# Performance work log

Measured on AMD Instinct MI355X. Metric: run time of the kernel, lower is better.

The kernel has to match this reference:

```python
import jax, jax.numpy as jnp
import numpy as np

B_, H_, N_, L_ = 4, 512, 64, 2048  # batch, d_model, d_state/2 (conj pairs), seq len


def setup_inputs() -> dict:
    key = jax.random.key(0)
    ks = jax.random.split(key, 8)
    x = jax.random.normal(ks[0], (B_, H_, L_), jnp.float32)
    ln_w = jnp.ones((H_,), jnp.float32)
    ln_b = jnp.zeros((H_,), jnp.float32)
    # S4D-style init: dt log-uniform in [1e-3, 1e-1], A = -1/2 + i*pi*n (S4D-Lin)
    log_dt = jax.random.uniform(ks[1], (H_,), jnp.float32) * (np.log(0.1) - np.log(0.001)) + np.log(0.001)
    log_A_real = jnp.broadcast_to(jnp.log(jnp.float32(0.5)), (H_, N_))
    A_imag = jnp.broadcast_to(np.pi * jnp.arange(N_, dtype=np.float32), (H_, N_))
    B_re = jnp.ones((H_, N_), jnp.float32)
    B_im = jnp.zeros((H_, N_), jnp.float32)
    # 2 kernel channels for bidirectional
    C_re = jax.random.normal(ks[2], (2, H_, N_), jnp.float32) * (0.5 ** 0.5)
    C_im = jax.random.normal(ks[3], (2, H_, N_), jnp.float32) * (0.5 ** 0.5)
    D = jax.random.normal(ks[4], (H_,), jnp.float32)
    W_out = jax.random.normal(ks[5], (H_, H_), jnp.float32) / np.sqrt(H_)
    b_out = jnp.zeros((H_,), jnp.float32)
    return dict(x=x, ln_w=ln_w, ln_b=ln_b, log_dt=log_dt, log_A_real=log_A_real,
                A_imag=A_imag, B_re=B_re, B_im=B_im, C_re=C_re, C_im=C_im,
                D=D, W_out=W_out, b_out=b_out)


def _s4_layer(x, ln_w, ln_b, log_dt, log_A_real, A_imag, B_re, B_im, C_re, C_im, D, W_out, b_out):
    Bb, H, L = x.shape
    # ---- pre-norm LayerNorm over channel dim (module transposes to (B,L,H)) ----
    zt = x.transpose(0, 2, 1)                          # (B, L, H)
    mu = zt.mean(-1, keepdims=True)
    var = jnp.mean((zt - mu) ** 2, -1, keepdims=True)
    zt = (zt - mu) * jax.lax.rsqrt(var + 1e-5) * ln_w + ln_b
    z = zt.transpose(0, 2, 1)                          # (B, H, L)
    # ---- S4 diagonal SSM kernel, ZOH discretization, 2 channels (bidirectional) ----
    dt = jnp.exp(log_dt)[:, None]                      # (H, 1)
    A = -jnp.exp(log_A_real) + 1j * A_imag             # (H, N)
    dtA = A * dt                                       # (H, N)
    dB = (B_re + 1j * B_im) * (jnp.exp(dtA) - 1.0) / A # (H, N) discretized B
    CB = (C_re + 1j * C_im) * dB                       # (2, H, N)
    V = jnp.exp(dtA[:, :, None] * jnp.arange(L))       # (H, N, L) Vandermonde exp(l*dt*A)
    k = 2.0 * jnp.real(jnp.einsum('chn,hnl->chl', CB, V))  # (2, H, L)
    # ---- bidirectional: causal + flipped anticausal kernel, length 2L ----
    zpad = jnp.zeros_like(k[0])
    kb = jnp.concatenate([k[0], zpad], -1) + jnp.concatenate([zpad, k[1][:, ::-1]], -1)  # (H, 2L)
    # ---- FFT convolution ----
    k_f = jnp.fft.rfft(kb, n=2 * L)                    # (H, L+1)
    u_f = jnp.fft.rfft(z, n=2 * L)                     # (B, H, L+1)
    y = jnp.fft.irfft(u_f * k_f, n=2 * L)[..., :L]     # (B, H, L)
    y = y + z * D[:, None]                             # skip connection D*u
    y = jax.nn.gelu(y)                                 # default S4 activation
    y = jnp.einsum('oh,bhl->bol', W_out, y) + b_out[:, None]  # output linear (Conv1d k=1)
    return y + x                                       # residual of S4Layer


def reference(x, ln_w, ln_b, log_dt, log_A_real, A_imag, B_re, B_im, C_re, C_im, D, W_out, b_out):
    return _s4_layer(x, ln_w, ln_b, log_dt, log_A_real, A_imag, B_re, B_im, C_re, C_im, D, W_out, b_out)
```

## Files before the change

kernel.cpp:

```cpp
#include <hip/hip_runtime.h>
#include <math.h>

#define Bq 4
#define Hq 512
#define Nq 64
#define Lq 2048
#define PARAM (Hq*Nq)

__global__ void prep_kernel(const float* __restrict__ log_dt,
                            const float* __restrict__ log_A_real,
                            const float* __restrict__ A_imag,
                            const float* __restrict__ B_re, const float* __restrict__ B_im,
                            const float* __restrict__ C_re, const float* __restrict__ C_im,
                            float* __restrict__ wr_, float* __restrict__ wi_,
                            float* __restrict__ a0, float* __restrict__ b0,
                            float* __restrict__ a1, float* __restrict__ b1) {
    int idx = blockIdx.x * blockDim.x + threadIdx.x;
    if (idx >= PARAM) return;
    int h = idx >> 6;
    float dt = expf(log_dt[h]);
    float Ar = -expf(log_A_real[idx]);
    float Ai = A_imag[idx];
    float er = expf(Ar * dt);
    float wr = er * cosf(Ai * dt);
    float wi = er * sinf(Ai * dt);
    wr_[idx] = wr; wi_[idx] = wi;
    float mr = wr - 1.0f, mi = wi;
    float den = Ar * Ar + Ai * Ai;
    float qr = (mr * Ar + mi * Ai) / den;
    float qi = (mi * Ar - mr * Ai) / den;
    float Br = B_re[idx], Bi = B_im[idx];
    float dBr = Br * qr - Bi * qi;
    float dBi = Br * qi + Bi * qr;
    float cr = C_re[idx], ci = C_im[idx];
    a0[idx] =  2.0f * (cr * dBr - ci * dBi);
    b0[idx] = -2.0f * (cr * dBi + ci * dBr);
    cr = C_re[PARAM + idx]; ci = C_im[PARAM + idx];
    a1[idx] =  2.0f * (cr * dBr - ci * dBi);
    b1[idx] = -2.0f * (cr * dBi + ci * dBr);
}

__global__ __launch_bounds__(256)
void ln_kernel(const float* __restrict__ x, const float* __restrict__ lnw,
               const float* __restrict__ lnb, float* __restrict__ z) {
    int blk = blockIdx.x;
    int b  = blk / (Lq / 16);
    int l0 = (blk % (Lq / 16)) * 16;
    int tx = threadIdx.x & 15;
    int ty = threadIdx.x >> 4;
    const float* xb = x + (size_t)b * Hq * Lq;
    float s = 0.f, s2 = 0.f;
    for (int h = ty; h < Hq; h += 16) {
        float v = xb[h * Lq + l0 + tx];
        s += v; s2 += v * v;
    }
    __shared__ float rs_[16][17], r2_[16][17], mu_s[16], sg_s[16];
    rs_[ty][tx] = s; r2_[ty][tx] = s2;
    __syncthreads();
    if (ty == 0) {
        float a = 0.f, c = 0.f;
        #pragma unroll
        for (int i = 0; i < 16; ++i) { a += rs_[i][tx]; c += r2_[i][tx]; }
        float mu = a * (1.0f / Hq);
        float var = c * (1.0f / Hq) - mu * mu;
        mu_s[tx] = mu;
        sg_s[tx] = rsqrtf(var + 1e-5f);
    }
    __syncthreads();
    float mu = mu_s[tx], rs = sg_s[tx];
    float* zb = z + (size_t)b * Hq * Lq;
    for (int h = ty; h < Hq; h += 16) {
        float v = xb[h * Lq + l0 + tx];
        zb[h * Lq + l0 + tx] = (v - mu) * rs * lnw[h] + lnb[h];
    }
}

template <int DIR>
__device__ __forceinline__ void scan_body(const float* __restrict__ zz,
                                          float* __restrict__ yout,
                                          float wr, float wi, float a, float b,
                                          float (*tile)[33], float* zbuf, int n) {
    float sr = 0.f, si = 0.f;
    for (int q0 = 0; q0 < Lq; q0 += 32) {
        if (n < 32) zbuf[n] = zz[DIR ? (Lq - 1 - q0 - n) : (q0 + n)];
        __syncthreads();
        float p[32];
        #pragma unroll
        for (int k = 0; k < 32; ++k) {
            float zt = zbuf[k];
            if (DIR == 0) {
                float t1 = fmaf(wi, si, -zt);
                float t2 = wi * sr;
                sr = fmaf(wr, sr, -t1);
                si = fmaf(wr, si, t2);
                p[k] = fmaf(a, sr, b * si);
            } else {
                p[k] = fmaf(a, sr, b * si);
                float t1 = fmaf(wi, si, -zt);
                float t2 = wi * sr;
                sr = fmaf(wr, sr, -t1);
                si = fmaf(wr, si, t2);
            }
        }
        #pragma unroll
        for (int k = 0; k < 32; ++k) tile[n][k] = p[k];
        __syncthreads();
        int tloc = n & 31, ih = n >> 5;
        float acc = 0.f;
        #pragma unroll
        for (int j = 0; j < 32; ++j) acc += tile[ih * 32 + j][tloc];
        acc += __shfl_xor(acc, 32, 64);
        if (n < 32) yout[DIR ? (Lq - 1 - q0 - n) : (q0 + n)] = acc;
    }
}

__global__ __launch_bounds__(64)
void scan_kernel(const float* __restrict__ z,
                 const float* __restrict__ wr_, const float* __restrict__ wi_,
                 const float* __restrict__ a0, const float* __restrict__ b0,
                 const float* __restrict__ a1, const float* __restrict__ b1,
                 float* __restrict__ y0, float* __restrict__ y1) {
    int bh  = blockIdx.x;
    int dir = blockIdx.y;
    int h = bh & (Hq - 1);
    int n = threadIdx.x;
    int pidx = h * Nq + n;
    float wr = wr_[pidx], wi = wi_[pidx];
    __shared__ float tile[64][33];
    __shared__ float zbuf[32];
    const float* zz = z + (size_t)bh * Lq;
    if (dir == 0) {
        scan_body<0>(zz, y0 + (size_t)bh * Lq, wr, wi, a0[pidx], b0[pidx], tile, zbuf, n);
    } else {
        scan_body<1>(zz, y1 + (size_t)bh * Lq, wr, wi, a1[pidx], b1[pidx], tile, zbuf, n);
    }
}

__global__ __launch_bounds__(256)
void act_kernel(float4* __restrict__ y0, const float4* __restrict__ y1,
                const float4* __restrict__ z, const float* __restrict__ D) {
    int i4 = blockIdx.x * 256 + threadIdx.x;
    int h = (i4 >> 9) & (Hq - 1);
    float d = D[h];
    float4 v0 = y0[i4], v1 = y1[i4], vz = z[i4];
    float vv[4] = { v0.x + v1.x + d * vz.x, v0.y + v1.y + d * vz.y,
                    v0.z + v1.z + d * vz.z, v0.w + v1.w + d * vz.w };
    #pragma unroll
    for (int i = 0; i < 4; ++i) {
        float v = vv[i];
        float t = tanhf(0.7978845608028654f * (v + 0.044715f * v * v * v));
        vv[i] = 0.5f * v * (1.0f + t);
    }
    float4 r; r.x = vv[0]; r.y = vv[1]; r.z = vv[2]; r.w = vv[3];
    y0[i4] = r;
}

__global__ __launch_bounds__(256)
void gemm_kernel(const float* __restrict__ u, const float* __restrict__ W,
                 const float* __restrict__ bias, const float* __restrict__ x,
                 float* __restrict__ out) {
    int l0 = blockIdx.x * 64;
    int o0 = blockIdx.y * 128;
    int b  = blockIdx.z;
    int tid = threadIdx.x;
    __shared__ float Ws[16][129];
    __shared__ float Us[16][65];
    const float* ub = u + (size_t)b * Hq * Lq;
    float acc[8][4] = {};
    int wo = tid >> 4, wl = tid & 15;
    for (int k0 = 0; k0 < Hq; k0 += 16) {
        {
            int j  = tid & 15;
            int ib = tid >> 4;
            #pragma unroll
            for (int r = 0; r < 8; ++r) {
                int i = ib + 16 * r;
                Ws[j][i] = W[(size_t)(o0 + i) * Hq + k0 + j];
            }
            int li = tid & 63;
            int jb = tid >> 6;
            #pragma unroll
            for (int r = 0; r < 4; ++r) {
                int j2 = jb + 4 * r;
                Us[j2][li] = ub[(size_t)(k0 + j2) * Lq + l0 + li];
            }
        }
        __syncthreads();
        #pragma unroll
        for (int j = 0; j < 16; ++j) {
            float av[8], bv[4];
            #pragma unroll
            for (int i = 0; i < 8; ++i) av[i] = Ws[j][8 * wo + i];
            #pragma unroll
            for (int i = 0; i < 4; ++i) bv[i] = Us[j][4 * wl + i];
            #pragma unroll
            for (int io = 0; io < 8; ++io)
                #pragma unroll
                for (int il = 0; il < 4; ++il)
                    acc[io][il] = fmaf(av[io], bv[il], acc[io][il]);
        }
        __syncthreads();
    }
    #pragma unroll
    for (int io = 0; io < 8; ++io) {
        int o = o0 + 8 * wo + io;
        float bo = bias[o];
        size_t base = ((size_t)b * Hq + o) * Lq + l0 + 4 * wl;
        const float4 xr = *(const float4*)(x + base);
        float4 r;
        r.x = acc[io][0] + bo + xr.x;
        r.y = acc[io][1] + bo + xr.y;
        r.z = acc[io][2] + bo + xr.z;
        r.w = acc[io][3] + bo + xr.w;
        *(float4*)(out + base) = r;
    }
}

extern "C" void kernel_launch(void* const* d_in, const int* in_sizes, int n_in,
                              void* d_out, int out_size, void* d_ws, size_t ws_size,
                              hipStream_t stream) {
    (void)in_sizes; (void)n_in; (void)out_size; (void)ws_size;
    const float* x          = (const float*)d_in[0];
    const float* ln_w       = (const float*)d_in[1];
    const float* ln_b       = (const float*)d_in[2];
    const float* log_dt     = (const float*)d_in[3];
    const float* log_A_real = (const float*)d_in[4];
    const float* A_imag     = (const float*)d_in[5];
    const float* B_re       = (const float*)d_in[6];
    const float* B_im       = (const float*)d_in[7];
    const float* C_re       = (const float*)d_in[8];
    const float* C_im       = (const float*)d_in[9];
    const float* Dv         = (const float*)d_in[10];
    const float* W          = (const float*)d_in[11];
    const float* b_out      = (const float*)d_in[12];
    float* out = (float*)d_out;
    float* ws  = (float*)d_ws;

    float* wr = ws;
    float* wi = ws + PARAM;
    float* a0 = ws + 2 * PARAM;
    float* b0 = ws + 3 * PARAM;
    float* a1 = ws + 4 * PARAM;
    float* b1 = ws + 5 * PARAM;
    float* z  = ws + 6 * PARAM;
    float* y0 = z  + (size_t)Bq * Hq * Lq;
    float* y1 = y0 + (size_t)Bq * Hq * Lq;

    prep_kernel<<<PARAM / 256, 256, 0, stream>>>(log_dt, log_A_real, A_imag,
                                                 B_re, B_im, C_re, C_im,
                                                 wr, wi, a0, b0, a1, b1);
    ln_kernel<<<Bq * (Lq / 16), 256, 0, stream>>>(x, ln_w, ln_b, z);
    scan_kernel<<<dim3(Bq * Hq, 2), 64, 0, stream>>>(z, wr, wi, a0, b0, a1, b1, y0, y1);
    act_kernel<<<(Bq * Hq * Lq / 4) / 256, 256, 0, stream>>>((float4*)y0, (const float4*)y1,
                                                             (const float4*)z, Dv);
    gemm_kernel<<<dim3(Lq / 64, Hq / 128, Bq), 256, 0, stream>>>(y0, W, b_out, x, out);
}
```

Before: 325.9 us.

## Chunk the SSM recurrence across sequence with a two-pass carry-combine scan

Splits each sequence into four chunks. A new local kernel computes the end state of each of the first three chunks, and the scan kernel combines those chunk states into carry-in states using precomputed powers w^512, w^1024 and w^1536, which are computed in double precision in the prep kernel. Each chunk's scan then runs in its own wavefront of a 256-thread block, which shortens the serial dependency chain by a factor of four and raises parallelism. The per-step reduction now uses wave-local LDS tiles with wave barriers instead of block syncs, and z is read directly with float4 loads. The cost is an extra kernel and a redundant pass over z, plus some precision risk when the chunk carries are combined.

After: 373.6 us. 1.15x slower.

```diff
diff --git a/kernel.cpp b/kernel.cpp
--- a/kernel.cpp
+++ b/kernel.cpp
@@ -6,6 +6,10 @@
 #define Nq 64
 #define Lq 2048
 #define PARAM (Hq*Nq)
+#define BH   (Bq*Hq)
+#define CCH  4
+#define LC   (Lq/CCH)
+static_assert(Lq == CCH*LC, "chunking");
 
 __global__ void prep_kernel(const float* __restrict__ log_dt,
                             const float* __restrict__ log_A_real,
@@ -14,7 +18,8 @@
                             const float* __restrict__ C_re, const float* __restrict__ C_im,
                             float* __restrict__ wr_, float* __restrict__ wi_,
                             float* __restrict__ a0, float* __restrict__ b0,
-                            float* __restrict__ a1, float* __restrict__ b1) {
+                            float* __restrict__ a1, float* __restrict__ b1,
+                            float* __restrict__ wpr, float* __restrict__ wpi) {
     int idx = blockIdx.x * blockDim.x + threadIdx.x;
     if (idx >= PARAM) return;
     int h = idx >> 6;
@@ -38,6 +43,18 @@
     cr = C_re[PARAM + idx]; ci = C_im[PARAM + idx];
     a1[idx] =  2.0f * (cr * dBr - ci * dBi);
     b1[idx] = -2.0f * (cr * dBi + ci * dBr);
+    double pr = (double)wr, pq = (double)wi;
+    #pragma unroll
+    for (int s = 0; s < 9; ++s) {
+        double nr = pr*pr - pq*pq;
+        double ni = 2.0*pr*pq;
+        pr = nr; pq = ni;
+    }
+    wpr[idx] = (float)pr;  wpi[idx] = (float)pq;
+    double p2r = pr*pr - pq*pq, p2i = 2.0*pr*pq;
+    wpr[PARAM + idx] = (float)p2r; wpi[PARAM + idx] = (float)p2i;
+    double p3r = p2r*pr - p2i*pq, p3i = p2r*pq + p2i*pr;
+    wpr[2*PARAM + idx] = (float)p3r; wpi[2*PARAM + idx] = (float)p3i;
 }
 
 __global__ __launch_bounds__(256)
@@ -75,65 +92,132 @@
     }
 }
 
+__device__ __forceinline__ void sstep(float& sr, float& si, float wr, float wi, float zt) {
+    float t1 = fmaf(wi, si, -zt);
+    float t2 = wi * sr;
+    sr = fmaf(wr, sr, -t1);
+    si = fmaf(wr, si, t2);
+}
+
+#define SSTEP4(qq)  do { sstep(sr,si,wr,wi,(qq).x); sstep(sr,si,wr,wi,(qq).y); \
+                         sstep(sr,si,wr,wi,(qq).z); sstep(sr,si,wr,wi,(qq).w); } while(0)
+#define SSTEP4R(qq) do { sstep(sr,si,wr,wi,(qq).w); sstep(sr,si,wr,wi,(qq).z); \
+                         sstep(sr,si,wr,wi,(qq).y); sstep(sr,si,wr,wi,(qq).x); } while(0)
+
+__global__ __launch_bounds__(256, 8)
+void local_kernel(const float* __restrict__ z,
+                  const float* __restrict__ wr_, const float* __restrict__ wi_,
+                  float* __restrict__ slocal) {
+    int wv = threadIdx.x >> 6;
+    int n  = threadIdx.x & 63;
+    int bh = blockIdx.x * 4 + wv;
+    int dir = blockIdx.y;
+    int c  = blockIdx.z;
+    int h  = bh & (Hq - 1);
+    int pidx = h * Nq + n;
+    float wr = wr_[pidx], wi = wi_[pidx];
+    const float* zz = z + (size_t)bh * Lq;
+    float sr = 0.f, si = 0.f;
+    int tau0 = c * LC;
+    if (dir == 0) {
+        const float4* zp = (const float4*)(zz + tau0);
+        for (int jj = 0; jj < LC; jj += 16) {
+            float4 q0 = zp[0], q1 = zp[1], q2 = zp[2], q3 = zp[3];
+            zp += 4;
+            SSTEP4(q0); SSTEP4(q1); SSTEP4(q2); SSTEP4(q3);
+        }
+    } else {
+        for (int jj = 0; jj < LC; jj += 16) {
+            const float4* zp = (const float4*)(zz + Lq - tau0 - jj - 16);
+            float4 q0 = zp[0], q1 = zp[1], q2 = zp[2], q3 = zp[3];
+            SSTEP4R(q3); SSTEP4R(q2); SSTEP4R(q1); SSTEP4R(q0);
+        }
+    }
+    float* out = slocal + ((size_t)(bh * 2 + dir) * (CCH - 1) + c) * 128;
+    out[n] = sr; out[64 + n] = si;
+}
+
 template <int DIR>
-__device__ __forceinline__ void scan_body(const float* __restrict__ zz,
-                                          float* __restrict__ yout,
-                                          float wr, float wi, float a, float b,
-                                          float (*tile)[33], float* zbuf, int n) {
-    float sr = 0.f, si = 0.f;
-    for (int q0 = 0; q0 < Lq; q0 += 32) {
-        if (n < 32) zbuf[n] = zz[DIR ? (Lq - 1 - q0 - n) : (q0 + n)];
-        __syncthreads();
-        float p[32];
+__device__ __forceinline__ void scan3_body(const float* __restrict__ zz,
+                                           float* __restrict__ yout,
+                                           float wr, float wi, float a, float b,
+                                           float sr, float si, int tau0, int n,
+                                           float (*tile)[17]) {
+    int g = n >> 4, tc = n & 15;
+    for (int q0 = 0; q0 < LC; q0 += 16) {
+        float4 q[4];
+        if (DIR == 0) {
+            const float4* zp = (const float4*)(zz + tau0 + q0);
+            q[0] = zp[0]; q[1] = zp[1]; q[2] = zp[2]; q[3] = zp[3];
+        } else {
+            const float4* zp = (const float4*)(zz + Lq - tau0 - q0 - 16);
+            q[0] = zp[0]; q[1] = zp[1]; q[2] = zp[2]; q[3] = zp[3];
+        }
         #pragma unroll
-        for (int k = 0; k < 32; ++k) {
-            float zt = zbuf[k];
+        for (int j = 0; j < 16; ++j) {
+            float zt;
             if (DIR == 0) {
-                float t1 = fmaf(wi, si, -zt);
-                float t2 = wi * sr;
-                sr = fmaf(wr, sr, -t1);
-                si = fmaf(wr, si, t2);
-                p[k] = fmaf(a, sr, b * si);
+                float4 qq = q[j >> 2];
+                zt = (j&3)==0 ? qq.x : (j&3)==1 ? qq.y : (j&3)==2 ? qq.z : qq.w;
             } else {
-                p[k] = fmaf(a, sr, b * si);
-                float t1 = fmaf(wi, si, -zt);
-                float t2 = wi * sr;
-                sr = fmaf(wr, sr, -t1);
-                si = fmaf(wr, si, t2);
+                float4 qq = q[3 - (j >> 2)];
+                zt = (j&3)==0 ? qq.w : (j&3)==1 ? qq.z : (j&3)==2 ? qq.y : qq.x;
             }
-        }
-        #pragma unroll
-        for (int k = 0; k < 32; ++k) tile[n][k] = p[k];
-        __syncthreads();
-        int tloc = n & 31, ih = n >> 5;
+            float p;
+            if (DIR == 0) { sstep(sr, si, wr, wi, zt); p = fmaf(a, sr, b * si); }
+            else          { p = fmaf(a, sr, b * si); sstep(sr, si, wr, wi, zt); }
+            tile[n][j] = p;
+        }
+        __builtin_amdgcn_wave_barrier();
         float acc = 0.f;
         #pragma unroll
-        for (int j = 0; j < 32; ++j) acc += tile[ih * 32 + j][tloc];
+        for (int r = 0; r < 16; ++r) acc += tile[g * 16 + r][tc];
+        acc += __shfl_xor(acc, 16, 64);
         acc += __shfl_xor(acc, 32, 64);
-        if (n < 32) yout[DIR ? (Lq - 1 - q0 - n) : (q0 + n)] = acc;
-    }
-}
-
-__global__ __launch_bounds__(64)
+        if (n < 16) {
+            int t = tau0 + q0 + n;
+            yout[DIR ? (Lq - 1 - t) : t] = acc;
+        }
+        __builtin_amdgcn_wave_barrier();
+    }
+}
+
+__global__ __launch_bounds__(256, 8)
 void scan_kernel(const float* __restrict__ z,
                  const float* __restrict__ wr_, const float* __restrict__ wi_,
                  const float* __restrict__ a0, const float* __restrict__ b0,
                  const float* __restrict__ a1, const float* __restrict__ b1,
+                 const float* __restrict__ wpr, const float* __restrict__ wpi,
+                 const float* __restrict__ slocal,
                  float* __restrict__ y0, float* __restrict__ y1) {
-    int bh  = blockIdx.x;
-    int dir = blockIdx.y;
+    __shared__ float tile[4][64][17];
+    int c = threadIdx.x >> 6;
+    int n = threadIdx.x & 63;
+    int bh = blockIdx.x, dir = blockIdx.y;
     int h = bh & (Hq - 1);
-    int n = threadIdx.x;
     int pidx = h * Nq + n;
     float wr = wr_[pidx], wi = wi_[pidx];
-    __shared__ float tile[64][33];
-    __shared__ float zbuf[32];
+    float sr = 0.f, si = 0.f;
+    const float* sl = slocal + (size_t)(bh * 2 + dir) * (CCH - 1) * 128;
+    for (int cp = 0; cp < c; ++cp) {
+        float lr = sl[cp * 128 + n], li = sl[cp * 128 + 64 + n];
+        int j = c - 1 - cp;
+        if (j == 0) { sr += lr; si += li; }
+        else {
+            float pr = wpr[(j - 1) * PARAM + pidx];
+            float pi = wpi[(j - 1) * PARAM + pidx];
+            sr += pr * lr - pi * li;
+            si += pr * li + pi * lr;
+        }
+    }
+    int tau0 = c * LC;
     const float* zz = z + (size_t)bh * Lq;
-    if (dir == 0) {
-        scan_body<0>(zz, y0 + (size_t)bh * Lq, wr, wi, a0[pidx], b0[pidx], tile, zbuf, n);
-    } else {
-        scan_body<1>(zz, y1 + (size_t)bh * Lq, wr, wi, a1[pidx], b1[pidx], tile, zbuf, n);
-    }
+    if (dir == 0)
+        scan3_body<0>(zz, y0 + (size_t)bh * Lq, wr, wi, a0[pidx], b0[pidx],
+                      sr, si, tau0, n, tile[c]);
+    else
+        scan3_body<1>(zz, y1 + (size_t)bh * Lq, wr, wi, a1[pidx], b1[pidx],
+                      sr, si, tau0, n, tile[c]);
 }
 
 __global__ __launch_bounds__(256)
@@ -236,21 +320,27 @@
     float* out = (float*)d_out;
     float* ws  = (float*)d_ws;
 
-    float* wr = ws;
-    float* wi = ws + PARAM;
-    float* a0 = ws + 2 * PARAM;
-    float* b0 = ws + 3 * PARAM;
-    float* a1 = ws + 4 * PARAM;
-    float* b1 = ws + 5 * PARAM;
-    float* z  = ws + 6 * PARAM;
-    float* y0 = z  + (size_t)Bq * Hq * Lq;
-    float* y1 = y0 + (size_t)Bq * Hq * Lq;
+    const size_t BHL = (size_t)Bq * Hq * Lq;
+    float* wr  = ws;
+    float* wi  = ws + PARAM;
+    float* a0  = ws + 2 * (size_t)PARAM;
+    float* b0  = ws + 3 * (size_t)PARAM;
+    float* a1  = ws + 4 * (size_t)PARAM;
+    float* b1  = ws + 5 * (size_t)PARAM;
+    float* wpr = ws + 6 * (size_t)PARAM;
+    float* wpi = ws + 9 * (size_t)PARAM;
+    float* z   = ws + 12 * (size_t)PARAM;
+    float* y0  = z  + BHL;
+    float* y1  = y0 + BHL;
+    float* slc = y1 + BHL;
 
     prep_kernel<<<PARAM / 256, 256, 0, stream>>>(log_dt, log_A_real, A_imag,
                                                  B_re, B_im, C_re, C_im,
-                                                 wr, wi, a0, b0, a1, b1);
+                                                 wr, wi, a0, b0, a1, b1, wpr, wpi);
     ln_kernel<<<Bq * (Lq / 16), 256, 0, stream>>>(x, ln_w, ln_b, z);
-    scan_kernel<<<dim3(Bq * Hq, 2), 64, 0, stream>>>(z, wr, wi, a0, b0, a1, b1, y0, y1);
+    local_kernel<<<dim3(BH / 4, 2, CCH - 1), 256, 0, stream>>>(z, wr, wi, slc);
+    scan_kernel<<<dim3(BH, 2), 256, 0, stream>>>(z, wr, wi, a0, b0, a1, b1,
+                                                 wpr, wpi, slc, y0, y1);
     act_kernel<<<(Bq * Hq * Lq / 4) / 256, 256, 0, stream>>>((float4*)y0, (const float4*)y1,
                                                              (const float4*)z, Dv);
     gemm_kernel<<<dim3(Lq / 64, Hq / 128, Bq), 256, 0, stream>>>(y0, W, b_out, x, out);
```

## Replace sequential SSM scan with chunked matmul-based scan

Applied to the files above, without the earlier changes.

Replaces the per-step recurrent scan over the full sequence with a chunked formulation. A delta kernel computes each chunk's state contribution as a matrix product with powers of the diagonal eigenvalues. A short inter-chunk scan then carries states across 32 chunks, and a y kernel combines the intra-chunk Toeplitz convolution with the carried-state contribution as a small GEMM. This removes the long serial dependency chain and exposes parallelism, at the cost of three kernel launches, an extra workspace buffer, and the numerical risk of power recurrences in float.

Measured after the change: 324.3 us. No clear change (-0.5%).

```diff
diff --git a/kernel.cpp b/kernel.cpp
--- a/kernel.cpp
+++ b/kernel.cpp
@@ -6,6 +6,9 @@
 #define Nq 64
 #define Lq 2048
 #define PARAM (Hq*Nq)
+#define T 64
+#define NC (Lq/T)
+#define NCOL 256
 
 __global__ void prep_kernel(const float* __restrict__ log_dt,
                             const float* __restrict__ log_A_real,
@@ -75,64 +78,238 @@
     }
 }
 
-template <int DIR>
-__device__ __forceinline__ void scan_body(const float* __restrict__ zz,
-                                          float* __restrict__ yout,
-                                          float wr, float wi, float a, float b,
-                                          float (*tile)[33], float* zbuf, int n) {
+
+__global__ __launch_bounds__(256)
+void delta_kernel(const float* __restrict__ z,
+                  const float* __restrict__ wr_, const float* __restrict__ wi_,
+                  float* __restrict__ buf) {
+    __shared__ float powc[64][64], pows[64][64];
+    __shared__ float Bs[64][68];
+    int h = blockIdx.x, ct = blockIdx.y;
+    int t = threadIdx.x;
+    if (t < 64) {
+        float wr = wr_[h*64+t], wi = wi_[h*64+t];
+        float c = 1.f, s = 0.f;
+        for (int d = 0; d < 64; ++d) {
+            powc[d][t] = c; pows[d][t] = s;
+            float nc = c*wr - s*wi, ns = c*wi + s*wr;
+            c = nc; s = ns;
+        }
+    }
+    {
+        int dir = ct >> 1;
+        int r = t >> 7, tt = t & 127;
+        int b = (ct & 1)*2 + r;
+        int l = tt * 16;
+        int c0 = l >> 6, j0 = l & 63;
+        const float* zb = z + ((size_t)b*Hq + h)*Lq;
+        int cc = r*32 + c0;
+        if (dir == 0) {
+            #pragma unroll
+            for (int q = 0; q < 4; ++q)
+                *(float4*)&Bs[cc][j0+4*q] = *(const float4*)(zb + c0*64 + j0 + 4*q);
+        } else {
+            #pragma unroll
+            for (int q = 0; q < 4; ++q) {
+                float4 v = *(const float4*)(zb + 2044 - c0*64 - (j0+4*q));
+                float4 w; w.x = v.w; w.y = v.z; w.z = v.y; w.w = v.x;
+                *(float4*)&Bs[cc][j0+4*q] = w;
+            }
+        }
+    }
+    __syncthreads();
+    int cg = t & 15, rg = t >> 4;
+    int n0 = 4*rg;
+    float aR[4][4] = {}, aI[4][4] = {};
+    #pragma unroll 4
+    for (int j = 0; j < 64; ++j) {
+        int d = 63 - j;
+        float4 pc = *(const float4*)&powc[d][n0];
+        float4 ps = *(const float4*)&pows[d][n0];
+        float bz[4];
+        #pragma unroll
+        for (int q = 0; q < 4; ++q) bz[q] = Bs[cg + 16*q][j];
+        #pragma unroll
+        for (int nn = 0; nn < 4; ++nn) {
+            float pcv = (&pc.x)[nn], psv = (&ps.x)[nn];
+            #pragma unroll
+            for (int q = 0; q < 4; ++q) {
+                aR[nn][q] = fmaf(pcv, bz[q], aR[nn][q]);
+                aI[nn][q] = fmaf(psv, bz[q], aI[nn][q]);
+            }
+        }
+    }
+    #pragma unroll
+    for (int q = 0; q < 4; ++q) {
+        int col = ct*64 + cg + 16*q;
+        float* dst = buf + ((size_t)h*NCOL + col)*128 + 2*n0;
+        float4 v1, v2;
+        v1.x = aR[0][q]; v1.y = aI[0][q]; v1.z = aR[1][q]; v1.w = aI[1][q];
+        v2.x = aR[2][q]; v2.y = aI[2][q]; v2.z = aR[3][q]; v2.w = aI[3][q];
+        *(float4*)dst = v1; *(float4*)(dst+4) = v2;
+    }
+}
+
+__global__ __launch_bounds__(256)
+void cscan_kernel(const float* __restrict__ wr_, const float* __restrict__ wi_,
+                  float* __restrict__ buf) {
+    int e = blockIdx.x*4 + (threadIdx.x >> 6);
+    int n = threadIdx.x & 63;
+    int h = e >> 3, dir = (e >> 2) & 1, b = e & 3;
+    float wr = wr_[h*64+n], wi = wi_[h*64+n];
+    double cr = wr, ci = wi;
+    #pragma unroll
+    for (int q = 0; q < 6; ++q) {
+        double nr = cr*cr - ci*ci, ni = 2.0*cr*ci;
+        cr = nr; ci = ni;
+    }
+    float tc = (float)cr, ts = (float)ci;
     float sr = 0.f, si = 0.f;
-    for (int q0 = 0; q0 < Lq; q0 += 32) {
-        if (n < 32) zbuf[n] = zz[DIR ? (Lq - 1 - q0 - n) : (q0 + n)];
+    float2* p = (float2*)(buf + ((size_t)h*NCOL + dir*128 + b*32)*128) + n;
+    float2 d = p[0];
+    for (int c = 0; c < NC; ++c) {
+        float2 dn;
+        if (c + 1 < NC) dn = p[(c+1)*64];
+        float2 s; s.x = sr; s.y = si;
+        p[c*64] = s;
+        float nr = fmaf(tc, sr, fmaf(-ts, si, d.x));
+        float ni = fmaf(ts, sr, fmaf(tc, si, d.y));
+        sr = nr; si = ni; d = dn;
+    }
+}
+
+__global__ __launch_bounds__(256)
+void y_kernel(const float* __restrict__ z,
+              const float* __restrict__ wr_, const float* __restrict__ wi_,
+              const float* __restrict__ a0, const float* __restrict__ b0,
+              const float* __restrict__ a1, const float* __restrict__ b1,
+              const float* __restrict__ buf,
+              float* __restrict__ y0, float* __restrict__ y1) {
+    __shared__ float powc[64][64], pows[64][64];
+    __shared__ float As[32][64];
+    __shared__ float Bs[64][36];
+    __shared__ float ks[64], as_[64], bs_[64];
+    int h = blockIdx.x, dir = blockIdx.y, ct = blockIdx.z;
+    int t = threadIdx.x;
+    const float* aa = dir ? a1 : a0;
+    const float* bb = dir ? b1 : b0;
+    if (t < 64) {
+        float wr = wr_[h*64+t], wi = wi_[h*64+t];
+        as_[t] = aa[h*64+t]; bs_[t] = bb[h*64+t];
+        float c, s;
+        if (dir == 0) { c = wr; s = wi; } else { c = 1.f; s = 0.f; }
+        for (int d = 0; d < 64; ++d) {
+            powc[d][t] = c; pows[d][t] = s;
+            float nc = c*wr - s*wi, ns = c*wi + s*wr;
+            c = nc; s = ns;
+        }
+    }
+    __syncthreads();
+    if (t < 64) {
+        int d = t;
+        float acc = 0.f;
+        if (dir == 0 && d == 0) {
+            for (int st = 0; st < 64; ++st) acc += as_[(st + d) & 63];
+        } else {
+            int row = (dir == 0) ? d - 1 : d;
+            for (int st = 0; st < 64; ++st) {
+                int n = (st + d) & 63;
+                acc = fmaf(as_[n], powc[row][n], acc);
+                acc = fmaf(bs_[n], pows[row][n], acc);
+            }
+        }
+        ks[d] = acc;
+    }
+    __syncthreads();
+    int tx = t & 15, ty = t >> 4;
+    float acc[4][4] = {};
+    for (int p = 0; p < 6; ++p) {
+        {
+            int kk = t & 31, ig = t >> 5;
+            if (p < 2) {
+                int j = 32*p + kk;
+                int off = (dir == 0) ? 0 : 1;
+                #pragma unroll
+                for (int ii = 0; ii < 8; ++ii) {
+                    int i = ig*8 + ii;
+                    int idx = i - j - off;
+                    As[kk][i] = (idx >= 0) ? ks[idx] : 0.f;
+                }
+            } else {
+                int m = 32*(p-2) + kk;
+                int n = m >> 1;
+                float av = as_[n], bv = bs_[n];
+                if ((m & 1) == 0) {
+                    #pragma unroll
+                    for (int ii = 0; ii < 8; ++ii) {
+                        int i = ig*8 + ii;
+                        As[kk][i] = fmaf(av, powc[i][n], bv*pows[i][n]);
+                    }
+                } else {
+                    #pragma unroll
+                    for (int ii = 0; ii < 8; ++ii) {
+                        int i = ig*8 + ii;
+                        As[kk][i] = fmaf(bv, powc[i][n], -av*pows[i][n]);
+                    }
+                }
+            }
+        }
+        {
+            int cc = t >> 2, q = t & 3;
+            int colg = ct*64 + cc;
+            int b = colg >> 5, c = colg & 31;
+            int kk0 = q*8;
+            if (p < 2) {
+                const float* zb = z + ((size_t)b*Hq + h)*Lq;
+                int j0 = 32*p + kk0;
+                if (dir == 0) {
+                    *(float4*)&Bs[cc][kk0]   = *(const float4*)(zb + c*64 + j0);
+                    *(float4*)&Bs[cc][kk0+4] = *(const float4*)(zb + c*64 + j0 + 4);
+                } else {
+                    float4 v = *(const float4*)(zb + 2044 - c*64 - j0);
+                    float4 w; w.x=v.w; w.y=v.z; w.z=v.y; w.w=v.x;
+                    *(float4*)&Bs[cc][kk0] = w;
+                    v = *(const float4*)(zb + 2044 - c*64 - (j0+4));
+                    w.x=v.w; w.y=v.z; w.z=v.y; w.w=v.x;
+                    *(float4*)&Bs[cc][kk0+4] = w;
+                }
+            } else {
+                int m0 = 32*(p-2) + kk0;
+                int col = dir*128 + colg;
+                const float* src = buf + ((size_t)h*NCOL + col)*128 + m0;
+                *(float4*)&Bs[cc][kk0]   = *(const float4*)src;
+                *(float4*)&Bs[cc][kk0+4] = *(const float4*)(src+4);
+            }
+        }
         __syncthreads();
-        float p[32];
-        #pragma unroll
-        for (int k = 0; k < 32; ++k) {
-            float zt = zbuf[k];
-            if (DIR == 0) {
-                float t1 = fmaf(wi, si, -zt);
-                float t2 = wi * sr;
-                sr = fmaf(wr, sr, -t1);
-                si = fmaf(wr, si, t2);
-                p[k] = fmaf(a, sr, b * si);
-            } else {
-                p[k] = fmaf(a, sr, b * si);
-                float t1 = fmaf(wi, si, -zt);
-                float t2 = wi * sr;
-                sr = fmaf(wr, sr, -t1);
-                si = fmaf(wr, si, t2);
-            }
-        }
-        #pragma unroll
-        for (int k = 0; k < 32; ++k) tile[n][k] = p[k];
+        #pragma unroll 8
+        for (int kk = 0; kk < 32; ++kk) {
+            float4 av = *(const float4*)&As[kk][4*tx];
+            float bv0 = Bs[4*ty+0][kk], bv1 = Bs[4*ty+1][kk];
+            float bv2 = Bs[4*ty+2][kk], bv3 = Bs[4*ty+3][kk];
+            #pragma unroll
+            for (int ii = 0; ii < 4; ++ii) {
+                float a = (&av.x)[ii];
+                acc[ii][0] = fmaf(a, bv0, acc[ii][0]);
+                acc[ii][1] = fmaf(a, bv1, acc[ii][1]);
+                acc[ii][2] = fmaf(a, bv2, acc[ii][2]);
+                acc[ii][3] = fmaf(a, bv3, acc[ii][3]);
+            }
+        }
         __syncthreads();
-        int tloc = n & 31, ih = n >> 5;
-        float acc = 0.f;
-        #pragma unroll
-        for (int j = 0; j < 32; ++j) acc += tile[ih * 32 + j][tloc];
-        acc += __shfl_xor(acc, 32, 64);
-        if (n < 32) yout[DIR ? (Lq - 1 - q0 - n) : (q0 + n)] = acc;
-    }
-}
-
-__global__ __launch_bounds__(64)
-void scan_kernel(const float* __restrict__ z,
-                 const float* __restrict__ wr_, const float* __restrict__ wi_,
-                 const float* __restrict__ a0, const float* __restrict__ b0,
-                 const float* __restrict__ a1, const float* __restrict__ b1,
-                 float* __restrict__ y0, float* __restrict__ y1) {
-    int bh  = blockIdx.x;
-    int dir = blockIdx.y;
-    int h = bh & (Hq - 1);
-    int n = threadIdx.x;
-    int pidx = h * Nq + n;
-    float wr = wr_[pidx], wi = wi_[pidx];
-    __shared__ float tile[64][33];
-    __shared__ float zbuf[32];
-    const float* zz = z + (size_t)bh * Lq;
-    if (dir == 0) {
-        scan_body<0>(zz, y0 + (size_t)bh * Lq, wr, wi, a0[pidx], b0[pidx], tile, zbuf, n);
-    } else {
-        scan_body<1>(zz, y1 + (size_t)bh * Lq, wr, wi, a1[pidx], b1[pidx], tile, zbuf, n);
+    }
+    #pragma unroll
+    for (int q = 0; q < 4; ++q) {
+        int colg = ct*64 + 4*ty + q;
+        int b = colg >> 5, c = colg & 31;
+        float4 v;
+        if (dir == 0) {
+            v.x = acc[0][q]; v.y = acc[1][q]; v.z = acc[2][q]; v.w = acc[3][q];
+            *(float4*)(y0 + ((size_t)b*Hq + h)*Lq + c*64 + 4*tx) = v;
+        } else {
+            v.x = acc[3][q]; v.y = acc[2][q]; v.z = acc[1][q]; v.w = acc[0][q];
+            *(float4*)(y1 + ((size_t)b*Hq + h)*Lq + 2044 - c*64 - 4*tx) = v;
+        }
     }
 }
 
@@ -148,8 +325,8 @@
     #pragma unroll
     for (int i = 0; i < 4; ++i) {
         float v = vv[i];
-        float t = tanhf(0.7978845608028654f * (v + 0.044715f * v * v * v));
-        vv[i] = 0.5f * v * (1.0f + t);
+        float tt = tanhf(0.7978845608028654f * (v + 0.044715f * v * v * v));
+        vv[i] = 0.5f * v * (1.0f + tt);
     }
     float4 r; r.x = vv[0]; r.y = vv[1]; r.z = vv[2]; r.w = vv[3];
     y0[i4] = r;
@@ -236,21 +413,26 @@
     float* out = (float*)d_out;
     float* ws  = (float*)d_ws;
 
-    float* wr = ws;
-    float* wi = ws + PARAM;
-    float* a0 = ws + 2 * PARAM;
-    float* b0 = ws + 3 * PARAM;
-    float* a1 = ws + 4 * PARAM;
-    float* b1 = ws + 5 * PARAM;
-    float* z  = ws + 6 * PARAM;
-    float* y0 = z  + (size_t)Bq * Hq * Lq;
-    float* y1 = y0 + (size_t)Bq * Hq * Lq;
+    const size_t BHL = (size_t)Bq * Hq * Lq;
+    float* wr  = ws;
+    float* wi  = ws + PARAM;
+    float* a0  = ws + 2 * (size_t)PARAM;
+    float* b0  = ws + 3 * (size_t)PARAM;
+    float* a1  = ws + 4 * (size_t)PARAM;
+    float* b1  = ws + 5 * (size_t)PARAM;
+    float* z   = ws + 6 * (size_t)PARAM;
+    float* y0  = z  + BHL;
+    float* y1  = y0 + BHL;
+    float* buf = y1 + BHL;
 
     prep_kernel<<<PARAM / 256, 256, 0, stream>>>(log_dt, log_A_real, A_imag,
                                                  B_re, B_im, C_re, C_im,
                                                  wr, wi, a0, b0, a1, b1);
     ln_kernel<<<Bq * (Lq / 16), 256, 0, stream>>>(x, ln_w, ln_b, z);
-    scan_kernel<<<dim3(Bq * Hq, 2), 64, 0, stream>>>(z, wr, wi, a0, b0, a1, b1, y0, y1);
+    delta_kernel<<<dim3(Hq, 4), 256, 0, stream>>>(z, wr, wi, buf);
+    cscan_kernel<<<Bq * Hq * 2 / 4, 256, 0, stream>>>(wr, wi, buf);
+    y_kernel<<<dim3(Hq, 2, 2), 256, 0, stream>>>(z, wr, wi, a0, b0, a1, b1,
+                                                 buf, y0, y1);
     act_kernel<<<(Bq * Hq * Lq / 4) / 256, 256, 0, stream>>>((float4*)y0, (const float4*)y1,
                                                              (const float4*)z, Dv);
     gemm_kernel<<<dim3(Lq / 64, Hq / 128, Bq), 256, 0, stream>>>(y0, W, b_out, x, out);
```
